# Kernel tuning notes

Hardware: AMD Instinct MI355X
Metric: run time of the kernel (lower is better)

The kernel has to match this reference:

```python
import jax, jax.numpy as jnp
import numpy as np

B, T, D = 1, 2048, 2048
HQ, HKV = 32, 8
DKV = 512  # HKV * head_dim

def setup_inputs() -> dict:
    key = jax.random.key(0)
    ks = jax.random.split(key, 5)
    s = 0.02
    return {
        "x": jax.random.normal(ks[0], (B, T, D), jnp.float32),
        "q_proj": jax.random.normal(ks[1], (D, D), jnp.float32) * s,
        "k_proj": jax.random.normal(ks[2], (DKV, D), jnp.float32) * s,
        "v_proj": jax.random.normal(ks[3], (DKV, D), jnp.float32) * s,
        "o_proj": jax.random.normal(ks[4], (D, D), jnp.float32) * s,
    }

def reference(x, q_proj, k_proj, v_proj, o_proj):
    b, t, _ = x.shape
    h_q, h_kv = HQ, HKV
    q_out = x @ q_proj.T            # [b,t,D]
    k_out = x @ k_proj.T            # [b,t,DKV]
    v_out = x @ v_proj.T
    dh_q = q_out.shape[-1] // h_q   # 64
    dh_k = k_out.shape[-1] // h_kv  # 64
    q = q_out.reshape(b, t, h_q, dh_q).transpose(0, 2, 1, 3)   # [b,hq,t,dh]
    k = k_out.reshape(b, t, h_kv, dh_k).transpose(0, 2, 1, 3)  # [b,hkv,t,dh]
    v = v_out.reshape(b, t, h_kv, dh_k).transpose(0, 2, 1, 3)
    group = h_q // h_kv
    k = jnp.repeat(k, group, axis=1)  # [b,hq,t,dh]
    v = jnp.repeat(v, group, axis=1)
    attn_logits = jnp.einsum('bhqd,bhkd->bhqk', q, k) / jnp.sqrt(jnp.float32(dh_q))
    mask = jnp.tril(jnp.ones((t, t), dtype=bool))
    attn = jax.nn.softmax(jnp.where(mask, attn_logits, -1e10), axis=-1)
    ctx = jnp.einsum('bhqk,bhkd->bhqd', attn, v)
    ctx = ctx.transpose(0, 2, 1, 3).reshape(b, t, o_proj.shape[0])
    return ctx @ o_proj
```

## Files before the change

### kernel.cpp

```cpp
#include <hip/hip_runtime.h>
#include <stdint.h>

typedef __attribute__((ext_vector_type(8))) __bf16 bf16x8;
typedef __attribute__((ext_vector_type(4))) float f32x4;
typedef __attribute__((ext_vector_type(4))) unsigned short u16x4;

typedef __attribute__((address_space(1))) unsigned int as1_uint;
typedef __attribute__((address_space(3))) unsigned int as3_uint;

__device__ __forceinline__ unsigned short f2bf(float f) {
  unsigned int u = __float_as_uint(f);
  u += 0x7fffu + ((u >> 16) & 1u);
  return (unsigned short)(u >> 16);
}

__device__ __forceinline__ void gload_lds16(const void* g, void* l) {
  __builtin_amdgcn_global_load_lds((as1_uint*)(uintptr_t)g, (as3_uint*)(uintptr_t)l,
                                   16, 0, 0);
}

__global__ void cvt_all(const float* __restrict__ x, const float* __restrict__ qp,
                        const float* __restrict__ kp, const float* __restrict__ vp,
                        unsigned short* __restrict__ xb, unsigned short* __restrict__ qpb,
                        unsigned short* __restrict__ kpb, unsigned short* __restrict__ vpb) {
  const int b = blockIdx.x;
  const float* in;
  unsigned short* out;
  int base;
  if (b < 4096)      { in = x;  out = xb;  base = b; }
  else if (b < 8192) { in = qp; out = qpb; base = b - 4096; }
  else if (b < 9216) { in = kp; out = kpb; base = b - 8192; }
  else               { in = vp; out = vpb; base = b - 9216; }
  const int i = base * 256 + threadIdx.x;
  float4 v = ((const float4*)in)[i];
  u16x4 o;
  o[0] = f2bf(v.x); o[1] = f2bf(v.y); o[2] = f2bf(v.z); o[3] = f2bf(v.w);
  ((u16x4*)out)[i] = o;
}

__global__ __launch_bounds__(256)
void transpose_cvt(const float* __restrict__ in, unsigned short* __restrict__ out,
                   int R, int C) {
  __shared__ unsigned short t[64][72];
  const int ti = blockIdx.y * 64;
  const int tj = blockIdx.x * 64;
  const int r  = threadIdx.x >> 4;
  const int c4 = (threadIdx.x & 15) * 4;
#pragma unroll
  for (int i = 0; i < 4; ++i) {
    int row = r + i * 16;
    float4 v = *(const float4*)&in[(size_t)(ti + row) * C + tj + c4];
    t[row][c4]     = f2bf(v.x);
    t[row][c4 + 1] = f2bf(v.y);
    t[row][c4 + 2] = f2bf(v.z);
    t[row][c4 + 3] = f2bf(v.w);
  }
  __syncthreads();
#pragma unroll
  for (int i = 0; i < 4; ++i) {
    int orow = r + i * 16;
    u16x4 o;
    o[0] = t[c4][orow]; o[1] = t[c4 + 1][orow];
    o[2] = t[c4 + 2][orow]; o[3] = t[c4 + 3][orow];
    *(u16x4*)&out[(size_t)(tj + orow) * R + ti + c4] = o;
  }
}

template <int BN, bool OUT_BF16>
__device__ __forceinline__
void gemm_body(const unsigned short* __restrict__ A,
               const unsigned short* __restrict__ B,
               void* __restrict__ Cout, int N, int K, float alpha,
               int bx, int by, unsigned short* lA, unsigned short* lB) {
  constexpr int NF  = BN / 32;
  constexpr int ASZ = 64 * 64;
  constexpr int BSZ = BN * 64;
  const int tid  = threadIdx.x;
  const int lane = tid & 63;
  const int w    = tid >> 6;
  const int wr   = (w >> 1) * 32;
  const int wc   = (w & 1) * (BN / 2);
  const long brow = (long)by * 64;
  const long bcol = (long)bx * BN;
  const int lr = lane & 15;
  const int lq = lane >> 4;

  const int row0 = tid >> 3;
  const int lc0  = (tid & 7) ^ (row0 & 7);

  f32x4 acc[2][NF] = {};

  const unsigned short* gA = A + (brow + row0) * (long)K + lc0 * 8;
  const unsigned short* gB = B + (bcol + row0) * (long)K + lc0 * 8;

#define G_STAGE(buf, k0)                                                          \
  {                                                                               \
    gload_lds16(gA + (k0),           lA + (buf) * ASZ + tid * 8);                 \
    gload_lds16(gA + 32l * K + (k0), lA + (buf) * ASZ + 2048 + tid * 8);          \
    _Pragma("unroll")                                                             \
    for (int g = 0; g < NF; ++g)                                                  \
      gload_lds16(gB + g * 32l * K + (k0), lB + (buf) * BSZ + g * 2048 + tid * 8);\
  }

  G_STAGE(0, 0);
  __syncthreads();

  for (int k0 = 0; k0 < K; k0 += 64) {
    const int cur = (k0 >> 6) & 1;
    if (k0 + 64 < K) G_STAGE(cur ^ 1, k0 + 64);
#pragma unroll
    for (int kk = 0; kk < 2; ++kk) {
      const int j = kk * 4 + lq;
      const int ra0 = wr + lr, ra1 = wr + 16 + lr;
      bf16x8 a0 = *(const bf16x8*)&lA[cur * ASZ + ra0 * 64 + ((j ^ (ra0 & 7)) << 3)];
      bf16x8 a1 = *(const bf16x8*)&lA[cur * ASZ + ra1 * 64 + ((j ^ (ra1 & 7)) << 3)];
      bf16x8 b[NF];
#pragma unroll
      for (int n = 0; n < NF; ++n) {
        const int rb = wc + n * 16 + lr;
        b[n] = *(const bf16x8*)&lB[cur * BSZ + rb * 64 + ((j ^ (rb & 7)) << 3)];
      }
#pragma unroll
      for (int n = 0; n < NF; ++n) {
        acc[0][n] = __builtin_amdgcn_mfma_f32_16x16x32_bf16(a0, b[n], acc[0][n], 0, 0, 0);
        acc[1][n] = __builtin_amdgcn_mfma_f32_16x16x32_bf16(a1, b[n], acc[1][n], 0, 0, 0);
      }
    }
    __syncthreads();
  }
#undef G_STAGE

  const int orow = (int)brow + wr + lq * 4;
  const int ocol = (int)bcol + wc + lr;
#pragma unroll
  for (int m = 0; m < 2; ++m)
#pragma unroll
    for (int n = 0; n < NF; ++n)
#pragma unroll
      for (int r = 0; r < 4; ++r) {
        size_t row = (size_t)(orow + m * 16 + r);
        size_t col = (size_t)(ocol + n * 16);
        float v = acc[m][n][r] * alpha;
        if (OUT_BF16)
          ((unsigned short*)Cout)[row * N + col] = f2bf(v);
        else
          ((float*)Cout)[row * N + col] = v;
      }
}

template <int BN, bool OUT_BF16>
__global__ __launch_bounds__(256)
void gemm_nt(const unsigned short* __restrict__ A,
             const unsigned short* __restrict__ B,
             void* __restrict__ Cout, int N, int K, float alpha) {
  __shared__ unsigned short lA[2 * 64 * 64];
  __shared__ unsigned short lB[2 * BN * 64];
  gemm_body<BN, OUT_BF16>(A, B, Cout, N, K, alpha, blockIdx.x, blockIdx.y, lA, lB);
}

__global__ __launch_bounds__(256)
void gemm_proj(const unsigned short* __restrict__ xb,
               const unsigned short* __restrict__ qpb,
               const unsigned short* __restrict__ kpb,
               const unsigned short* __restrict__ vpb,
               unsigned short* __restrict__ Qb, unsigned short* __restrict__ Kbf,
               unsigned short* __restrict__ Vtb) {
  __shared__ unsigned short lA[2 * 64 * 64];
  __shared__ unsigned short lB[2 * 128 * 64];
  const int bid = blockIdx.x;
  const unsigned short *A, *B;
  unsigned short* C;
  int N, bx, by;
  float alpha;
  if (bid < 512) {
    A = xb;  B = qpb; C = Qb;  N = 2048; alpha = 0.125f * 1.44269504088896f;
    bx = bid & 15; by = bid >> 4;
  } else if (bid < 640) {
    int b = bid - 512;
    A = xb;  B = kpb; C = Kbf; N = 512;  alpha = 1.0f;
    bx = b & 3; by = b >> 2;
  } else {
    int b = bid - 640;
    A = vpb; B = xb;  C = Vtb; N = 2048; alpha = 1.0f;
    bx = b & 15; by = b >> 4;
  }
  gemm_body<128, true>(A, B, C, N, 2048, alpha, bx, by, lA, lB);
}

__global__ __launch_bounds__(256)
void attn64(const unsigned short* __restrict__ Q,
            const unsigned short* __restrict__ Kb,
            const unsigned short* __restrict__ Vt,
            unsigned short* __restrict__ ctx) {
  constexpr int T = 2048, DQ = 2048, DKV = 512, DH = 64;
  const int h    = blockIdx.x;
  const int hkv  = h >> 2;
  const int tid  = threadIdx.x;
  const int lane = tid & 63;
  const int w    = tid >> 6;
  const int lr   = lane & 15;
  const int lq   = lane >> 4;
  const int lk   = lq * 8;
  const int sw   = lr & 7;

  __shared__ unsigned short lK[3][64 * 64];
  __shared__ unsigned short lV[3][64 * 64];
  __shared__ unsigned short P[4][16][72];

  const int row0 = tid >> 3;
  const int lc0  = (tid & 7) ^ (row0 & 7);

  bf16x8 ones_frag;
#pragma unroll
  for (int i = 0; i < 8; ++i) ones_frag[i] = (lr == 0) ? (__bf16)1.0f : (__bf16)0.0f;

#define STAGE_KV(bufidx, kv0)                                                        \
  {                                                                                  \
    gload_lds16(Kb + (size_t)((kv0) + row0) * DKV + hkv * DH + lc0 * 8,              \
                &lK[bufidx][tid * 8]);                                               \
    gload_lds16(Kb + (size_t)((kv0) + row0 + 32) * DKV + hkv * DH + lc0 * 8,         \
                &lK[bufidx][2048 + tid * 8]);                                        \
    gload_lds16(Vt + (size_t)(hkv * DH + row0) * T + (kv0) + lc0 * 8,                \
                &lV[bufidx][tid * 8]);                                               \
    gload_lds16(Vt + (size_t)(hkv * DH + row0 + 32) * T + (kv0) + lc0 * 8,           \
                &lV[bufidx][2048 + tid * 8]);                                        \
  }

#pragma unroll 1
  for (int pass = 0; pass < 2; ++pass) {
    const int qi  = pass == 0 ? (int)blockIdx.y : 31 - (int)blockIdx.y;
    const int q0b = qi * 64;
    const int qw  = q0b + w * 16;

    bf16x8 qf0 = *(const bf16x8*)&Q[(size_t)(qw + lr) * DQ + h * DH + lk];
    bf16x8 qf1 = *(const bf16x8*)&Q[(size_t)(qw + lr) * DQ + h * DH + 32 + lk];

    f32x4 oacc[4] = {};
    f32x4 lacc = {};
    float mr[4];
#pragma unroll
    for (int r = 0; r < 4; ++r) mr[r] = -3.0e38f;

    const int nt = qi + 1;
    STAGE_KV(0, 0);
    if (nt > 1) {
      STAGE_KV(1, 64);
      asm volatile("s_waitcnt vmcnt(4)" ::: "memory");
    } else {
      asm volatile("s_waitcnt vmcnt(0)" ::: "memory");
    }
    __builtin_amdgcn_sched_barrier(0);
    __builtin_amdgcn_s_barrier();

    for (int t = 0; t < nt; ++t) {
      const int kv0 = t * 64;
      const int cur = t % 3;
      const bool more = (t + 2 < nt);
      if (more) STAGE_KV((t + 2) % 3, kv0 + 128);

      f32x4 s[4];
      __builtin_amdgcn_s_setprio(1);
#pragma unroll
      for (int n = 0; n < 4; ++n) {
        const int krow = n * 16 + lr;
        bf16x8 kf0 = *(const bf16x8*)&lK[cur][krow * 64 + ((lq ^ sw) << 3)];
        bf16x8 kf1 = *(const bf16x8*)&lK[cur][krow * 64 + (((4 + lq) ^ sw) << 3)];
        f32x4 acc = {};
        acc = __builtin_amdgcn_mfma_f32_16x16x32_bf16(qf0, kf0, acc, 0, 0, 0);
        acc = __builtin_amdgcn_mfma_f32_16x16x32_bf16(qf1, kf1, acc, 0, 0, 0);
        s[n] = acc;
      }
      __builtin_amdgcn_s_setprio(0);

      if (t == qi) {
        const int qr0 = qw + (lq << 2);
#pragma unroll
        for (int n = 0; n < 4; ++n) {
          int kc = kv0 + n * 16 + lr;
#pragma unroll
          for (int r = 0; r < 4; ++r)
            if (kc > qr0 + r) s[n][r] = -3.0e38f;
        }
      }

      float lml[4];
#pragma unroll
      for (int r = 0; r < 4; ++r)
        lml[r] = fmaxf(fmaxf(s[0][r], s[1][r]), fmaxf(s[2][r], s[3][r]));
      const bool defer = __all((lml[0] <= mr[0] + 8.f) & (lml[1] <= mr[1] + 8.f) &
                               (lml[2] <= mr[2] + 8.f) & (lml[3] <= mr[3] + 8.f));
      if (!defer) {
#pragma unroll
        for (int r = 0; r < 4; ++r) {
          float ml = lml[r];
          ml = fmaxf(ml, __shfl_xor(ml, 1));
          ml = fmaxf(ml, __shfl_xor(ml, 2));
          ml = fmaxf(ml, __shfl_xor(ml, 4));
          ml = fmaxf(ml, __shfl_xor(ml, 8));
          float mnew = fmaxf(mr[r], ml);
          float sc   = __builtin_amdgcn_exp2f(mr[r] - mnew);
          mr[r] = mnew;
          lacc[r] *= sc;
          oacc[0][r] *= sc; oacc[1][r] *= sc;
          oacc[2][r] *= sc; oacc[3][r] *= sc;
        }
      }

#pragma unroll
      for (int n = 0; n < 4; ++n)
#pragma unroll
        for (int r = 0; r < 4; ++r)
          s[n][r] = __builtin_amdgcn_exp2f(s[n][r] - mr[r]);

#pragma unroll
      for (int n = 0; n < 4; ++n)
#pragma unroll
        for (int r = 0; r < 4; ++r)
          P[w][(lq << 2) + r][n * 16 + lr] =
              (unsigned short)(__float_as_uint(s[n][r]) >> 16);
      asm volatile("s_waitcnt lgkmcnt(0)" ::: "memory");
      __builtin_amdgcn_sched_barrier(0);

      __builtin_amdgcn_s_setprio(1);
#pragma unroll
      for (int ks = 0; ks < 2; ++ks) {
        bf16x8 pf = *(const bf16x8*)&P[w][lr][ks * 32 + lk];
        lacc = __builtin_amdgcn_mfma_f32_16x16x32_bf16(pf, ones_frag, lacc, 0, 0, 0);
#pragma unroll
        for (int n = 0; n < 4; ++n) {
          const int vrow = n * 16 + lr;
          bf16x8 vf = *(const bf16x8*)&lV[cur][vrow * 64 + (((ks * 4 + lq) ^ sw) << 3)];
          oacc[n] = __builtin_amdgcn_mfma_f32_16x16x32_bf16(pf, vf, oacc[n], 0, 0, 0);
        }
      }
      __builtin_amdgcn_s_setprio(0);

      if (more) asm volatile("s_waitcnt vmcnt(4)" ::: "memory");
      else      asm volatile("s_waitcnt vmcnt(0)" ::: "memory");
      __builtin_amdgcn_sched_barrier(0);
      __builtin_amdgcn_s_barrier();
    }

    float inv[4];
#pragma unroll
    for (int r = 0; r < 4; ++r) {
      float l = __shfl(lacc[r], lane & 48);
      inv[r] = 1.f / l;
    }
#pragma unroll
    for (int n = 0; n < 4; ++n)
#pragma unroll
      for (int r = 0; r < 4; ++r) {
        int qrow = qw + (lq << 2) + r;
        ctx[(size_t)qrow * DQ + h * DH + n * 16 + lr] = f2bf(oacc[n][r] * inv[r]);
      }
  }
#undef STAGE_KV
}

extern "C" void kernel_launch(void* const* d_in, const int* in_sizes, int n_in,
                              void* d_out, int out_size, void* d_ws, size_t ws_size,
                              hipStream_t stream) {
  const float* x  = (const float*)d_in[0];
  const float* qp = (const float*)d_in[1];
  const float* kp = (const float*)d_in[2];
  const float* vp = (const float*)d_in[3];
  const float* op = (const float*)d_in[4];

  char* ws = (char*)d_ws;
  const size_t MB = 1024 * 1024;
  unsigned short* xb   = (unsigned short*)(ws + 0 * MB);
  unsigned short* qpb  = (unsigned short*)(ws + 8 * MB);
  unsigned short* kpb  = (unsigned short*)(ws + 16 * MB);
  unsigned short* vpb  = (unsigned short*)(ws + 18 * MB);
  unsigned short* opT  = (unsigned short*)(ws + 20 * MB);
  unsigned short* Qb   = (unsigned short*)(ws + 28 * MB);
  unsigned short* Kbf  = (unsigned short*)(ws + 36 * MB);
  unsigned short* Vtb  = (unsigned short*)(ws + 38 * MB);
  unsigned short* ctxb = (unsigned short*)(ws + 40 * MB);

  cvt_all<<<10240, 256, 0, stream>>>(x, qp, kp, vp, xb, qpb, kpb, vpb);
  transpose_cvt<<<dim3(32, 32), 256, 0, stream>>>(op, opT, 2048, 2048);

  gemm_proj<<<768, 256, 0, stream>>>(xb, qpb, kpb, vpb, Qb, Kbf, Vtb);

  attn64<<<dim3(32, 16), 256, 0, stream>>>(Qb, Kbf, Vtb, ctxb);

  gemm_nt<128, false><<<dim3(16, 32), 256, 0, stream>>>(ctxb, opT, d_out, 2048, 2048, 1.0f);
}
```

Measured before the change: 116.9 us.

## Split attention q-tiles into separate blocks with double-buffered KV and occupancy hint

Each attention block now processes one 64-row query tile instead of two paired tiles, so the grid doubles to 1024 blocks. A snake ordering over blockIdx.y keeps the causal work balanced. KV staging drops from triple to double buffering, and the P tile loses its padding in favour of an XOR swizzle, which cuts LDS use so launch_bounds(256,4) can fit more blocks per CU. The cost is a shallower prefetch pipeline, full __syncthreads in place of the hand-tuned waitcnt/barrier, and possibly more register pressure.

```diff
diff --git a/kernel.cpp b/kernel.cpp
--- a/kernel.cpp
+++ b/kernel.cpp
@@ -187,7 +187,7 @@
   gemm_body<128, true>(A, B, C, N, 2048, alpha, bx, by, lA, lB);
 }
 
-__global__ __launch_bounds__(256)
+__global__ __launch_bounds__(256, 4)
 void attn64(const unsigned short* __restrict__ Q,
             const unsigned short* __restrict__ Kb,
             const unsigned short* __restrict__ Vt,
@@ -195,6 +195,9 @@
   constexpr int T = 2048, DQ = 2048, DKV = 512, DH = 64;
   const int h    = blockIdx.x;
   const int hkv  = h >> 2;
+  const int ya   = blockIdx.y >> 3;
+  const int yb   = blockIdx.y & 7;
+  const int qi   = (ya == 0) ? yb : (ya == 1) ? 15 - yb : (ya == 2) ? 16 + yb : 31 - yb;
   const int tid  = threadIdx.x;
   const int lane = tid & 63;
   const int w    = tid >> 6;
@@ -203,9 +206,9 @@
   const int lk   = lq * 8;
   const int sw   = lr & 7;
 
-  __shared__ unsigned short lK[3][64 * 64];
-  __shared__ unsigned short lV[3][64 * 64];
-  __shared__ unsigned short P[4][16][72];
+  __shared__ unsigned short lK[2][64 * 64];
+  __shared__ unsigned short lV[2][64 * 64];
+  __shared__ unsigned short P[4][16][64];
 
   const int row0 = tid >> 3;
   const int lc0  = (tid & 7) ^ (row0 & 7);
@@ -226,135 +229,122 @@
                 &lV[bufidx][2048 + tid * 8]);                                        \
   }
 
-#pragma unroll 1
-  for (int pass = 0; pass < 2; ++pass) {
-    const int qi  = pass == 0 ? (int)blockIdx.y : 31 - (int)blockIdx.y;
-    const int q0b = qi * 64;
-    const int qw  = q0b + w * 16;
-
-    bf16x8 qf0 = *(const bf16x8*)&Q[(size_t)(qw + lr) * DQ + h * DH + lk];
-    bf16x8 qf1 = *(const bf16x8*)&Q[(size_t)(qw + lr) * DQ + h * DH + 32 + lk];
-
-    f32x4 oacc[4] = {};
-    f32x4 lacc = {};
-    float mr[4];
-#pragma unroll
-    for (int r = 0; r < 4; ++r) mr[r] = -3.0e38f;
-
-    const int nt = qi + 1;
-    STAGE_KV(0, 0);
-    if (nt > 1) {
-      STAGE_KV(1, 64);
-      asm volatile("s_waitcnt vmcnt(4)" ::: "memory");
-    } else {
-      asm volatile("s_waitcnt vmcnt(0)" ::: "memory");
-    }
+  const int q0b = qi * 64;
+  const int qw  = q0b + w * 16;
+
+  bf16x8 qf0 = *(const bf16x8*)&Q[(size_t)(qw + lr) * DQ + h * DH + lk];
+  bf16x8 qf1 = *(const bf16x8*)&Q[(size_t)(qw + lr) * DQ + h * DH + 32 + lk];
+
+  f32x4 oacc[4] = {};
+  f32x4 lacc = {};
+  float mr[4];
+#pragma unroll
+  for (int r = 0; r < 4; ++r) mr[r] = -3.0e38f;
+
+  const int nt = qi + 1;
+  STAGE_KV(0, 0);
+  __syncthreads();
+
+  for (int t = 0; t < nt; ++t) {
+    const int kv0 = t * 64;
+    const int cur = t & 1;
+    if (t + 1 < nt) STAGE_KV(cur ^ 1, kv0 + 64);
+
+    f32x4 s[4];
+    __builtin_amdgcn_s_setprio(1);
+#pragma unroll
+    for (int n = 0; n < 4; ++n) {
+      const int krow = n * 16 + lr;
+      bf16x8 kf0 = *(const bf16x8*)&lK[cur][krow * 64 + ((lq ^ sw) << 3)];
+      bf16x8 kf1 = *(const bf16x8*)&lK[cur][krow * 64 + (((4 + lq) ^ sw) << 3)];
+      f32x4 acc = {};
+      acc = __builtin_amdgcn_mfma_f32_16x16x32_bf16(qf0, kf0, acc, 0, 0, 0);
+      acc = __builtin_amdgcn_mfma_f32_16x16x32_bf16(qf1, kf1, acc, 0, 0, 0);
+      s[n] = acc;
+    }
+    __builtin_amdgcn_s_setprio(0);
+
+    if (t == qi) {
+      const int qr0 = qw + (lq << 2);
+#pragma unroll
+      for (int n = 0; n < 4; ++n) {
+        int kc = kv0 + n * 16 + lr;
+#pragma unroll
+        for (int r = 0; r < 4; ++r)
+          if (kc > qr0 + r) s[n][r] = -3.0e38f;
+      }
+    }
+
+    float lml[4];
+#pragma unroll
+    for (int r = 0; r < 4; ++r)
+      lml[r] = fmaxf(fmaxf(s[0][r], s[1][r]), fmaxf(s[2][r], s[3][r]));
+    const bool defer = __all((lml[0] <= mr[0] + 8.f) & (lml[1] <= mr[1] + 8.f) &
+                             (lml[2] <= mr[2] + 8.f) & (lml[3] <= mr[3] + 8.f));
+    if (!defer) {
+#pragma unroll
+      for (int r = 0; r < 4; ++r) {
+        float ml = lml[r];
+        ml = fmaxf(ml, __shfl_xor(ml, 1));
+        ml = fmaxf(ml, __shfl_xor(ml, 2));
+        ml = fmaxf(ml, __shfl_xor(ml, 4));
+        ml = fmaxf(ml, __shfl_xor(ml, 8));
+        float mnew = fmaxf(mr[r], ml);
+        float sc   = __builtin_amdgcn_exp2f(mr[r] - mnew);
+        mr[r] = mnew;
+        lacc[r] *= sc;
+        oacc[0][r] *= sc; oacc[1][r] *= sc;
+        oacc[2][r] *= sc; oacc[3][r] *= sc;
+      }
+    }
+
+#pragma unroll
+    for (int n = 0; n < 4; ++n)
+#pragma unroll
+      for (int r = 0; r < 4; ++r)
+        s[n][r] = __builtin_amdgcn_exp2f(s[n][r] - mr[r]);
+
+#pragma unroll
+    for (int n = 0; n < 4; ++n)
+#pragma unroll
+      for (int r = 0; r < 4; ++r) {
+        const int prow = (lq << 2) + r;
+        P[w][prow][(((2 * n + (lr >> 3)) ^ (prow & 7)) << 3) + (lr & 7)] =
+            (unsigned short)(__float_as_uint(s[n][r]) >> 16);
+      }
+    asm volatile("s_waitcnt lgkmcnt(0)" ::: "memory");
     __builtin_amdgcn_sched_barrier(0);
-    __builtin_amdgcn_s_barrier();
-
-    for (int t = 0; t < nt; ++t) {
-      const int kv0 = t * 64;
-      const int cur = t % 3;
-      const bool more = (t + 2 < nt);
-      if (more) STAGE_KV((t + 2) % 3, kv0 + 128);
-
-      f32x4 s[4];
-      __builtin_amdgcn_s_setprio(1);
+
+    __builtin_amdgcn_s_setprio(1);
+#pragma unroll
+    for (int ks = 0; ks < 2; ++ks) {
+      bf16x8 pf = *(const bf16x8*)&P[w][lr][((ks * 4 + lq) ^ sw) << 3];
+      lacc = __builtin_amdgcn_mfma_f32_16x16x32_bf16(pf, ones_frag, lacc, 0, 0, 0);
 #pragma unroll
       for (int n = 0; n < 4; ++n) {
-        const int krow = n * 16 + lr;
-        bf16x8 kf0 = *(const bf16x8*)&lK[cur][krow * 64 + ((lq ^ sw) << 3)];
-        bf16x8 kf1 = *(const bf16x8*)&lK[cur][krow * 64 + (((4 + lq) ^ sw) << 3)];
-        f32x4 acc = {};
-        acc = __builtin_amdgcn_mfma_f32_16x16x32_bf16(qf0, kf0, acc, 0, 0, 0);
-        acc = __builtin_amdgcn_mfma_f32_16x16x32_bf16(qf1, kf1, acc, 0, 0, 0);
-        s[n] = acc;
-      }
-      __builtin_amdgcn_s_setprio(0);
-
-      if (t == qi) {
-        const int qr0 = qw + (lq << 2);
-#pragma unroll
-        for (int n = 0; n < 4; ++n) {
-          int kc = kv0 + n * 16 + lr;
-#pragma unroll
-          for (int r = 0; r < 4; ++r)
-            if (kc > qr0 + r) s[n][r] = -3.0e38f;
-        }
-      }
-
-      float lml[4];
-#pragma unroll
-      for (int r = 0; r < 4; ++r)
-        lml[r] = fmaxf(fmaxf(s[0][r], s[1][r]), fmaxf(s[2][r], s[3][r]));
-      const bool defer = __all((lml[0] <= mr[0] + 8.f) & (lml[1] <= mr[1] + 8.f) &
-                               (lml[2] <= mr[2] + 8.f) & (lml[3] <= mr[3] + 8.f));
-      if (!defer) {
-#pragma unroll
-        for (int r = 0; r < 4; ++r) {
-          float ml = lml[r];
-          ml = fmaxf(ml, __shfl_xor(ml, 1));
-          ml = fmaxf(ml, __shfl_xor(ml, 2));
-          ml = fmaxf(ml, __shfl_xor(ml, 4));
-          ml = fmaxf(ml, __shfl_xor(ml, 8));
-          float mnew = fmaxf(mr[r], ml);
-          float sc   = __builtin_amdgcn_exp2f(mr[r] - mnew);
-          mr[r] = mnew;
-          lacc[r] *= sc;
-          oacc[0][r] *= sc; oacc[1][r] *= sc;
-          oacc[2][r] *= sc; oacc[3][r] *= sc;
-        }
-      }
-
-#pragma unroll
-      for (int n = 0; n < 4; ++n)
-#pragma unroll
-        for (int r = 0; r < 4; ++r)
-          s[n][r] = __builtin_amdgcn_exp2f(s[n][r] - mr[r]);
-
-#pragma unroll
-      for (int n = 0; n < 4; ++n)
-#pragma unroll
-        for (int r = 0; r < 4; ++r)
-          P[w][(lq << 2) + r][n * 16 + lr] =
-              (unsigned short)(__float_as_uint(s[n][r]) >> 16);
-      asm volatile("s_waitcnt lgkmcnt(0)" ::: "memory");
-      __builtin_amdgcn_sched_barrier(0);
-
-      __builtin_amdgcn_s_setprio(1);
-#pragma unroll
-      for (int ks = 0; ks < 2; ++ks) {
-        bf16x8 pf = *(const bf16x8*)&P[w][lr][ks * 32 + lk];
-        lacc = __builtin_amdgcn_mfma_f32_16x16x32_bf16(pf, ones_frag, lacc, 0, 0, 0);
-#pragma unroll
-        for (int n = 0; n < 4; ++n) {
-          const int vrow = n * 16 + lr;
-          bf16x8 vf = *(const bf16x8*)&lV[cur][vrow * 64 + (((ks * 4 + lq) ^ sw) << 3)];
-          oacc[n] = __builtin_amdgcn_mfma_f32_16x16x32_bf16(pf, vf, oacc[n], 0, 0, 0);
-        }
-      }
-      __builtin_amdgcn_s_setprio(0);
-
-      if (more) asm volatile("s_waitcnt vmcnt(4)" ::: "memory");
-      else      asm volatile("s_waitcnt vmcnt(0)" ::: "memory");
-      __builtin_amdgcn_sched_barrier(0);
-      __builtin_amdgcn_s_barrier();
-    }
-
-    float inv[4];
+        const int vrow = n * 16 + lr;
+        bf16x8 vf = *(const bf16x8*)&lV[cur][vrow * 64 + (((ks * 4 + lq) ^ sw) << 3)];
+        oacc[n] = __builtin_amdgcn_mfma_f32_16x16x32_bf16(pf, vf, oacc[n], 0, 0, 0);
+      }
+    }
+    __builtin_amdgcn_s_setprio(0);
+
+    __syncthreads();
+  }
+
+  float inv[4];
+#pragma unroll
+  for (int r = 0; r < 4; ++r) {
+    float l = __shfl(lacc[r], lane & 48);
+    inv[r] = 1.f / l;
+  }
+#pragma unroll
+  for (int n = 0; n < 4; ++n)
 #pragma unroll
     for (int r = 0; r < 4; ++r) {
-      float l = __shfl(lacc[r], lane & 48);
-      inv[r] = 1.f / l;
-    }
-#pragma unroll
-    for (int n = 0; n < 4; ++n)
-#pragma unroll
-      for (int r = 0; r < 4; ++r) {
-        int qrow = qw + (lq << 2) + r;
-        ctx[(size_t)qrow * DQ + h * DH + n * 16 + lr] = f2bf(oacc[n][r] * inv[r]);
-      }
-  }
+      int qrow = qw + (lq << 2) + r;
+      ctx[(size_t)qrow * DQ + h * DH + n * 16 + lr] = f2bf(oacc[n][r] * inv[r]);
+    }
 #undef STAGE_KV
 }
 
@@ -384,7 +374,7 @@
 
   gemm_proj<<<768, 256, 0, stream>>>(xb, qpb, kpb, vpb, Qb, Kbf, Vtb);
 
-  attn64<<<dim3(32, 16), 256, 0, stream>>>(Qb, Kbf, Vtb, ctxb);
+  attn64<<<dim3(32, 32), 256, 0, stream>>>(Qb, Kbf, Vtb, ctxb);
 
   gemm_nt<128, false><<<dim3(16, 32), 256, 0, stream>>>(ctxb, opT, d_out, 2048, 2048, 1.0f);
 }
```

New measurement: 113.8 us. 2.6% less time.
